# Optimization experiments

Hardware: AMD Instinct MI355X
Metric: run time of the kernel (lower is better)

The kernel has to match this reference:

```python
import jax, jax.numpy as jnp
import numpy as np

B, T, S, D = 4, 4, 128, 256  # batch, turns, seq_len, hidden_size
H = D  # GRU units == hidden_size


def setup_inputs() -> dict:
    key = jax.random.key(0)
    ks = jax.random.split(key, 8)
    sc = lambda *sh: float(np.sqrt(2.0 / sum(sh[:2]))) if len(sh) > 1 else 0.05
    return {
        "features": jax.random.normal(ks[0], (B, T, S, D), jnp.float32),
        "w1": jax.random.normal(ks[1], (D, D), jnp.float32) * sc(D, D),
        "w2": jax.random.normal(ks[2], (D, D), jnp.float32) * sc(D, D),
        "bias": jax.random.normal(ks[3], (D,), jnp.float32) * 0.05,
        "v3": jax.random.normal(ks[4], (D,), jnp.float32) * 0.05,
        "gru_kernel": jax.random.normal(ks[5], (2 * D, 3 * H), jnp.float32) * sc(2 * D, 3 * H),
        "gru_rec_kernel": jax.random.normal(ks[6], (H, 3 * H), jnp.float32) * sc(H, 3 * H),
        "gru_bias": jax.random.normal(ks[7], (2, 3 * H), jnp.float32) * 0.05,
    }


def _gru(x, kernel, rec_kernel, bias):
    # x: [N, S, 2D]; Keras GRU (reset_after=True, tanh/sigmoid), h0 = 0.
    b_in, b_rec = bias[0], bias[1]
    xp = x @ kernel + b_in               # [N, S, 3H] input projections
    xp_t = jnp.swapaxes(xp, 0, 1)        # [S, N, 3H]
    h0 = jnp.zeros((x.shape[0], H), x.dtype)

    def step(h, xt):
        rp = h @ rec_kernel + b_rec      # [N, 3H]
        xz, xr, xh = jnp.split(xt, 3, axis=-1)
        rz, rr, rh = jnp.split(rp, 3, axis=-1)
        z = jax.nn.sigmoid(xz + rz)
        r = jax.nn.sigmoid(xr + rr)
        hh = jnp.tanh(xh + r * rh)
        h_new = z * h + (1.0 - z) * hh
        return h_new, h_new

    _, ys = jax.lax.scan(step, h0, xp_t)  # ys: [S, N, H]
    return jnp.swapaxes(ys, 0, 1)         # [N, S, H]


def reference(features, w1, w2, bias, v3, gru_kernel, gru_rec_kernel, gru_bias):
    b, t, s, d = features.shape
    x = features.reshape(b * t, s, d)     # fold turns into batch (same per-utterance math)
    left = jnp.einsum('bsd,dt->bst', x, w1)
    right = jnp.einsum('bsd,dt->bst', x, w2)
    # additive (Bahdanau) scores: [N, s, s, d] intermediate
    temp = jnp.tanh(left[:, :, None, :] + right[:, None, :, :] + bias)
    score = jax.nn.softmax(jnp.einsum('bmnd,d->bmn', temp, v3), axis=-1)
    c = jnp.einsum('bmn,bnd->bmd', score, x)
    p = _gru(jnp.concatenate([x, c], axis=-1), gru_kernel, gru_rec_kernel, gru_bias)
    return p.reshape(b, t, s, H)
```

## Files before the change

kernel.cpp:

```cpp
#include <hip/hip_runtime.h>
#include <hip/hip_bf16.h>

typedef __attribute__((ext_vector_type(8))) short short8;
typedef __attribute__((ext_vector_type(4))) float floatx4;

#define NSEQ 16
#define SEQ 128
#define DIM 256
#define HID 256
#define K3H 768
#define K2D 512
#define LOG2E 1.442695041f
#define LOG2E2 2.885390082f
#define WS_STRIDE 772

__device__ __forceinline__ float frcp(float x) { return __builtin_amdgcn_rcpf(x); }
__device__ __forceinline__ unsigned short bf16bits(float v) {
    unsigned u = __builtin_bit_cast(unsigned, v);
    unsigned r = (u + 0x7FFFu + ((u >> 16) & 1u)) >> 16;
    return (unsigned short)r;
}
__device__ __forceinline__ void load_lds16(const float* gsrc, float* ldsbase) {
    __builtin_amdgcn_global_load_lds(
        (const __attribute__((address_space(1))) void*)gsrc,
        (__attribute__((address_space(3))) void*)ldsbase, 16, 0, 0);
}

__global__ __launch_bounds__(256) void k1_leftright(
        const float* __restrict__ x, const float* __restrict__ w1,
        const float* __restrict__ w2, float* __restrict__ left,
        float* __restrict__ right) {
    __shared__ __align__(16) float xs[8][DIM];
    const int tid = threadIdx.x;
    const int r0 = blockIdx.x * 8;
    #pragma unroll
    for (int i = 0; i < 8; ++i) xs[i][tid] = x[(r0 + i) * DIM + tid];
    __syncthreads();
    float accL[8], accR[8];
    #pragma unroll
    for (int i = 0; i < 8; ++i) { accL[i] = 0.f; accR[i] = 0.f; }
    #pragma unroll 4
    for (int d = 0; d < DIM; ++d) {
        float wa = w1[d * DIM + tid];
        float wb = w2[d * DIM + tid];
        #pragma unroll
        for (int i = 0; i < 8; ++i) {
            float xv = xs[i][d];
            accL[i] = fmaf(xv, wa, accL[i]);
            accR[i] = fmaf(xv, wb, accR[i]);
        }
    }
    #pragma unroll
    for (int i = 0; i < 8; ++i) {
        left[(r0 + i) * DIM + tid]  = accL[i] * LOG2E2;
        right[(r0 + i) * DIM + tid] = accR[i] * LOG2E2;
    }
}

__global__ __launch_bounds__(256) void k2_attn(
        const float* __restrict__ x, const float* __restrict__ left,
        const float* __restrict__ right, const float* __restrict__ bias,
        const float* __restrict__ v3, float* __restrict__ cout) {
    __shared__ __align__(16) float lm[8][DIM];
    __shared__ __align__(16) float v3s[DIM];
    __shared__ __align__(16) float P[8][SEQ];
    const int tid = threadIdx.x;
    const int b  = blockIdx.x >> 4;
    const int m0 = (blockIdx.x & 15) * 8;

    v3s[tid & 255] = v3[tid & 255];
    #pragma unroll
    for (int i = 0; i < 8; ++i)
        lm[i][tid] = left[(size_t)(b * SEQ + m0 + i) * DIM + tid] + bias[tid] * LOG2E2;
    __syncthreads();

    const int mi = tid >> 5;
    const int nl = tid & 31;
    float sacc[4] = {0.f, 0.f, 0.f, 0.f};
    const float4* lv4 = reinterpret_cast<const float4*>(lm[mi]);
    const float4* vv4 = reinterpret_cast<const float4*>(v3s);
    #pragma unroll 2
    for (int d4 = 0; d4 < DIM / 4; ++d4) {
        float4 lv = lv4[d4];
        float4 vv = vv4[d4];
        #pragma unroll
        for (int rep = 0; rep < 4; ++rep) {
            const int n = nl + rep * 32;
            float4 rv = reinterpret_cast<const float4*>(right + (size_t)(b * SEQ + n) * DIM)[d4];
            float t0 = 1.f - 2.f * frcp(1.f + __builtin_amdgcn_exp2f(lv.x + rv.x));
            float t1 = 1.f - 2.f * frcp(1.f + __builtin_amdgcn_exp2f(lv.y + rv.y));
            float t2 = 1.f - 2.f * frcp(1.f + __builtin_amdgcn_exp2f(lv.z + rv.z));
            float t3 = 1.f - 2.f * frcp(1.f + __builtin_amdgcn_exp2f(lv.w + rv.w));
            sacc[rep] = fmaf(t0, vv.x, sacc[rep]);
            sacc[rep] = fmaf(t1, vv.y, sacc[rep]);
            sacc[rep] = fmaf(t2, vv.z, sacc[rep]);
            sacc[rep] = fmaf(t3, vv.w, sacc[rep]);
        }
    }
    #pragma unroll
    for (int rep = 0; rep < 4; ++rep) P[mi][nl + rep * 32] = sacc[rep];
    __syncthreads();

    {
        const int w   = tid >> 6;
        const int lane = tid & 63;
        const int row = w * 2 + (lane >> 5);
        const int g   = lane & 31;
        float v0 = P[row][g], v1 = P[row][g + 32], v2 = P[row][g + 64], v3v = P[row][g + 96];
        float mx = fmaxf(fmaxf(v0, v1), fmaxf(v2, v3v));
        #pragma unroll
        for (int off = 16; off >= 1; off >>= 1) mx = fmaxf(mx, __shfl_xor(mx, off, 64));
        float e0 = __expf(v0 - mx), e1 = __expf(v1 - mx);
        float e2 = __expf(v2 - mx), e3 = __expf(v3v - mx);
        float sm = e0 + e1 + e2 + e3;
        #pragma unroll
        for (int off = 16; off >= 1; off >>= 1) sm += __shfl_xor(sm, off, 64);
        float inv = frcp(sm);
        P[row][g] = e0 * inv; P[row][g + 32] = e1 * inv;
        P[row][g + 64] = e2 * inv; P[row][g + 96] = e3 * inv;
    }
    __syncthreads();

    float acc[8];
    #pragma unroll
    for (int i = 0; i < 8; ++i) acc[i] = 0.f;
    const float* xb = x + (size_t)b * SEQ * DIM;
    for (int nc = 0; nc < SEQ / 4; ++nc) {
        float xv0 = xb[(nc * 4 + 0) * DIM + tid];
        float xv1 = xb[(nc * 4 + 1) * DIM + tid];
        float xv2 = xb[(nc * 4 + 2) * DIM + tid];
        float xv3 = xb[(nc * 4 + 3) * DIM + tid];
        #pragma unroll
        for (int i = 0; i < 8; ++i) {
            float4 pv = *reinterpret_cast<const float4*>(&P[i][nc * 4]);
            acc[i] = fmaf(pv.x, xv0, acc[i]);
            acc[i] = fmaf(pv.y, xv1, acc[i]);
            acc[i] = fmaf(pv.z, xv2, acc[i]);
            acc[i] = fmaf(pv.w, xv3, acc[i]);
        }
    }
    #pragma unroll
    for (int i = 0; i < 8; ++i)
        cout[(size_t)(b * SEQ + m0 + i) * DIM + tid] = acc[i];
}

__global__ __launch_bounds__(512) void k3_mfma(
        const float* __restrict__ x, const float* __restrict__ c,
        const float* __restrict__ gk, const float* __restrict__ gbias,
        float* __restrict__ xp) {
    __shared__ __align__(16) unsigned short As[64][72];
    __shared__ __align__(16) unsigned short Bs[192][72];
    const int tid  = threadIdx.x;
    const int lane = tid & 63;
    const int w    = tid >> 6;
    const int l15  = lane & 15;
    const int g4   = lane >> 4;
    const int wm   = w >> 2;
    const int wn   = w & 3;
    const int m0   = (blockIdx.x & 31) * 64;
    const int n0   = (blockIdx.x >> 5) * 192;

    floatx4 Cf[2][3];
    #pragma unroll
    for (int i = 0; i < 2; ++i)
        #pragma unroll
        for (int j = 0; j < 3; ++j) Cf[i][j] = (floatx4){0.f, 0.f, 0.f, 0.f};

    for (int ch = 0; ch < 8; ++ch) {
        const int kbase = ch * 64;
        #pragma unroll
        for (int q = 0; q < 2; ++q) {
            int fi = q * 512 + tid;
            int row = fi >> 4, kq = (fi & 15) << 2;
            int kg = kbase + kq;
            const float* src = (kg < 256) ? &x[(size_t)(m0 + row) * DIM + kg]
                                          : &c[(size_t)(m0 + row) * DIM + (kg - 256)];
            float4 v = *reinterpret_cast<const float4*>(src);
            unsigned short* dst = &As[row][kq];
            dst[0] = bf16bits(v.x); dst[1] = bf16bits(v.y);
            dst[2] = bf16bits(v.z); dst[3] = bf16bits(v.w);
        }
        #pragma unroll
        for (int q = 0; q < 6; ++q) {
            int fi = q * 512 + tid;
            int krow = fi / 48, nq = (fi % 48) << 2;
            float4 v = *reinterpret_cast<const float4*>(
                &gk[(size_t)(kbase + krow) * K3H + n0 + nq]);
            Bs[nq + 0][krow] = bf16bits(v.x);
            Bs[nq + 1][krow] = bf16bits(v.y);
            Bs[nq + 2][krow] = bf16bits(v.z);
            Bs[nq + 3][krow] = bf16bits(v.w);
        }
        __syncthreads();
        #pragma unroll
        for (int kk = 0; kk < 2; ++kk) {
            short8 af[2], bf[3];
            #pragma unroll
            for (int i = 0; i < 2; ++i)
                af[i] = *reinterpret_cast<const short8*>(&As[wm * 32 + i * 16 + l15][kk * 32 + g4 * 8]);
            #pragma unroll
            for (int j = 0; j < 3; ++j)
                bf[j] = *reinterpret_cast<const short8*>(&Bs[wn * 48 + j * 16 + l15][kk * 32 + g4 * 8]);
            #pragma unroll
            for (int i = 0; i < 2; ++i)
                #pragma unroll
                for (int j = 0; j < 3; ++j)
                    Cf[i][j] = __builtin_amdgcn_mfma_f32_16x16x32_bf16(af[i], bf[j], Cf[i][j], 0, 0, 0);
        }
        __syncthreads();
    }

    #pragma unroll
    for (int j = 0; j < 3; ++j) {
        const int nbase = n0 + wn * 48 + j * 16;
        const int col = nbase + l15;
        const float sc = (nbase >= 512) ? LOG2E2 : LOG2E;
        const float bv = ((col < 512) ? (gbias[col] + gbias[K3H + col]) : gbias[col]) * sc;
        #pragma unroll
        for (int i = 0; i < 2; ++i) {
            const int rbase = m0 + wm * 32 + i * 16 + g4 * 4;
            #pragma unroll
            for (int r = 0; r < 4; ++r)
                xp[(size_t)(rbase + r) * K3H + col] = fmaf(Cf[i][j][r], sc, bv);
        }
    }
}

__global__ __launch_bounds__(512) void k4_gru(
        const float* __restrict__ rec, const float* __restrict__ gbias,
        const float* __restrict__ xp, float* __restrict__ out) {
    __shared__ __align__(16) float ws[16 * WS_STRIDE];
    __shared__ __align__(16) float xq[3][K3H];
    __shared__ __align__(16) unsigned short hbf[2][HID];
    const int tid  = threadIdx.x;
    const int lane = tid & 63;
    const int wv   = tid >> 6;
    const int seq  = blockIdx.x;
    const int l15  = lane & 15;
    const int g4   = lane >> 4;

    short8 Bf[6][8];
    #pragma unroll
    for (int part = 0; part < 16; ++part) {
        #pragma unroll
        for (int q = 0; q < 6; ++q) {
            int fi = q * 512 + tid;
            int row = fi / 192, c4 = fi % 192;
            reinterpret_cast<float4*>(ws)[row * (WS_STRIDE / 4) + c4] =
                reinterpret_cast<const float4*>(rec + part * 16 * K3H)[fi];
        }
        __syncthreads();
        const int kc = part >> 1, half = part & 1;
        #pragma unroll
        for (int u = 0; u < 6; ++u) {
            const float sc = (u >= 4) ? LOG2E2 : LOG2E;
            const int col = (u >> 1) * 256 + (u & 1) * 16 + wv * 32 + l15;
            #pragma unroll
            for (int j = 0; j < 8; ++j) {
                int r = g4 * 8 + j;
                if ((r >> 4) == half)
                    Bf[u][kc][j] = (short)bf16bits(ws[(r & 15) * WS_STRIDE + col] * sc);
            }
        }
        __syncthreads();
    }

    const int dd = wv * 32 + (lane & 31);
    const float brh_l = gbias[K3H + 512 + dd] * LOG2E2;
    const int tsel = (lane >> 4) & 1;

    const float* xps = xp + (size_t)seq * SEQ * K3H;
    float* outs = out + (size_t)seq * SEQ * HID;

    float h = 0.f;
    if (tid < HID) hbf[0][tid] = 0;

    if (wv < 3) {
        load_lds16(xps + wv * 256 + (lane << 2),       &xq[0][wv * 256]);
        load_lds16(xps + K3H + wv * 256 + (lane << 2), &xq[1][wv * 256]);
    }
    asm volatile("s_waitcnt vmcnt(0)" ::: "memory");
    __syncthreads();

    int bc = 0, bn2 = 2;
    for (int s = 0; s < SEQ; ++s) {
        const int cb = s & 1, nb = cb ^ 1;

        const int sp = (s + 2 < SEQ) ? s + 2 : SEQ - 1;
        if (wv < 3)
            load_lds16(xps + (size_t)sp * K3H + wv * 256 + (lane << 2), &xq[bn2][wv * 256]);

        short8 av[8];
        #pragma unroll
        for (int kc = 0; kc < 8; ++kc)
            av[kc] = *reinterpret_cast<const short8*>(&hbf[cb][kc * 32 + g4 * 8]);
        const float xz = xq[bc][dd];
        const float xr = xq[bc][256 + dd];
        const float xh = xq[bc][512 + dd];

        floatx4 C[6];
        #pragma unroll
        for (int u = 0; u < 6; ++u) C[u] = (floatx4){0.f, 0.f, 0.f, 0.f};
        #pragma unroll
        for (int kc = 0; kc < 8; ++kc) {
            #pragma unroll
            for (int u = 0; u < 6; ++u)
                C[u] = __builtin_amdgcn_mfma_f32_16x16x32_bf16(av[kc], Bf[u][kc], C[u], 0, 0, 0);
        }
        if (lane < 32) {
            float rz = tsel ? C[1][0] : C[0][0];
            float rr = tsel ? C[3][0] : C[2][0];
            float rh = tsel ? C[5][0] : C[4][0];
            float z  = frcp(1.f + __builtin_amdgcn_exp2f(-(rz + xz)));
            float r  = frcp(1.f + __builtin_amdgcn_exp2f(-(rr + xr)));
            float th = fmaf(r, rh + brh_l, xh);
            float hh = 1.f - 2.f * frcp(1.f + __builtin_amdgcn_exp2f(th));
            h = hh + z * (h - hh);
            hbf[nb][dd] = bf16bits(h);
            outs[s * HID + dd] = h;
        }
        asm volatile("s_waitcnt vmcnt(3) lgkmcnt(0)\n\ts_barrier" ::: "memory");

        bc  = (bc == 2)  ? 0 : bc + 1;
        bn2 = (bn2 == 2) ? 0 : bn2 + 1;
    }
}

extern "C" void kernel_launch(void* const* d_in, const int* in_sizes, int n_in,
                              void* d_out, int out_size, void* d_ws, size_t ws_size,
                              hipStream_t stream) {
    const float* feat = (const float*)d_in[0];
    const float* w1   = (const float*)d_in[1];
    const float* w2   = (const float*)d_in[2];
    const float* bias = (const float*)d_in[3];
    const float* v3   = (const float*)d_in[4];
    const float* gk   = (const float*)d_in[5];
    const float* grk  = (const float*)d_in[6];
    const float* gb   = (const float*)d_in[7];
    float* out = (float*)d_out;

    char* wsb = (char*)d_ws;
    float* left  = (float*)(wsb);
    float* right = (float*)(wsb + (size_t)2 * 1024 * 1024);
    float* cbuf  = (float*)(wsb + (size_t)4 * 1024 * 1024);
    float* xp    = (float*)(wsb + (size_t)6 * 1024 * 1024);

    k1_leftright<<<2048 / 8, 256, 0, stream>>>(feat, w1, w2, left, right);
    k2_attn<<<NSEQ * 16, 256, 0, stream>>>(feat, left, right, bias, v3, cbuf);
    k3_mfma<<<128, 512, 0, stream>>>(feat, cbuf, gk, gb, xp);
    k4_gru<<<NSEQ, 512, 0, stream>>>(grk, gb, xp, out);
}
```

Before: 241.9 us.

## Process two GRU sequences per block to interleave independent recurrences

The GRU kernel now handles two sequences per workgroup, launching half as many blocks. Each step runs two independent MFMA chains on the same register-resident recurrent weights, so one sequence's latency can be hidden behind the other's. The per-step critical path grows, since each wave issues twice the MFMAs and activations, and only 8 blocks run on a large GPU, which lowers parallelism. The wait count is adjusted for the extra outstanding stores and loads per step.

```diff
diff --git a/kernel.cpp b/kernel.cpp
--- a/kernel.cpp
+++ b/kernel.cpp
@@ -230,12 +230,13 @@
         const float* __restrict__ rec, const float* __restrict__ gbias,
         const float* __restrict__ xp, float* __restrict__ out) {
     __shared__ __align__(16) float ws[16 * WS_STRIDE];
-    __shared__ __align__(16) float xq[3][K3H];
-    __shared__ __align__(16) unsigned short hbf[2][HID];
+    __shared__ __align__(16) float xqA[3][K3H];
+    __shared__ __align__(16) float xqB[3][K3H];
+    __shared__ __align__(16) unsigned short hbfA[2][HID];
+    __shared__ __align__(16) unsigned short hbfB[2][HID];
     const int tid  = threadIdx.x;
     const int lane = tid & 63;
     const int wv   = tid >> 6;
-    const int seq  = blockIdx.x;
     const int l15  = lane & 15;
     const int g4   = lane >> 4;
 
@@ -269,15 +270,22 @@
     const float brh_l = gbias[K3H + 512 + dd] * LOG2E2;
     const int tsel = (lane >> 4) & 1;
 
-    const float* xps = xp + (size_t)seq * SEQ * K3H;
-    float* outs = out + (size_t)seq * SEQ * HID;
-
-    float h = 0.f;
-    if (tid < HID) hbf[0][tid] = 0;
+    const int sA = blockIdx.x * 2, sB = sA + 1;
+    const float* xpsA = xp + (size_t)sA * SEQ * K3H;
+    const float* xpsB = xp + (size_t)sB * SEQ * K3H;
+    float* outsA = out + (size_t)sA * SEQ * HID;
+    float* outsB = out + (size_t)sB * SEQ * HID;
+
+    float hA = 0.f, hB = 0.f;
+    if (tid < HID) { hbfA[0][tid] = 0; hbfB[0][tid] = 0; }
 
     if (wv < 3) {
-        load_lds16(xps + wv * 256 + (lane << 2),       &xq[0][wv * 256]);
-        load_lds16(xps + K3H + wv * 256 + (lane << 2), &xq[1][wv * 256]);
+        load_lds16(xpsA + wv * 256 + (lane << 2),       &xqA[0][wv * 256]);
+        load_lds16(xpsA + K3H + wv * 256 + (lane << 2), &xqA[1][wv * 256]);
+    } else if (wv < 6) {
+        const int w3 = wv - 3;
+        load_lds16(xpsB + w3 * 256 + (lane << 2),       &xqB[0][w3 * 256]);
+        load_lds16(xpsB + K3H + w3 * 256 + (lane << 2), &xqB[1][w3 * 256]);
     }
     asm volatile("s_waitcnt vmcnt(0)" ::: "memory");
     __syncthreads();
@@ -288,38 +296,68 @@
 
         const int sp = (s + 2 < SEQ) ? s + 2 : SEQ - 1;
         if (wv < 3)
-            load_lds16(xps + (size_t)sp * K3H + wv * 256 + (lane << 2), &xq[bn2][wv * 256]);
-
-        short8 av[8];
+            load_lds16(xpsA + (size_t)sp * K3H + wv * 256 + (lane << 2), &xqA[bn2][wv * 256]);
+        else if (wv < 6)
+            load_lds16(xpsB + (size_t)sp * K3H + (wv - 3) * 256 + (lane << 2), &xqB[bn2][(wv - 3) * 256]);
+
+        short8 avA[8];
         #pragma unroll
         for (int kc = 0; kc < 8; ++kc)
-            av[kc] = *reinterpret_cast<const short8*>(&hbf[cb][kc * 32 + g4 * 8]);
-        const float xz = xq[bc][dd];
-        const float xr = xq[bc][256 + dd];
-        const float xh = xq[bc][512 + dd];
-
-        floatx4 C[6];
-        #pragma unroll
-        for (int u = 0; u < 6; ++u) C[u] = (floatx4){0.f, 0.f, 0.f, 0.f};
+            avA[kc] = *reinterpret_cast<const short8*>(&hbfA[cb][kc * 32 + g4 * 8]);
+        const float xzA = xqA[bc][dd];
+        const float xrA = xqA[bc][256 + dd];
+        const float xhA = xqA[bc][512 + dd];
+        floatx4 CA[6];
+        #pragma unroll
+        for (int u = 0; u < 6; ++u) CA[u] = (floatx4){0.f, 0.f, 0.f, 0.f};
         #pragma unroll
         for (int kc = 0; kc < 8; ++kc) {
             #pragma unroll
             for (int u = 0; u < 6; ++u)
-                C[u] = __builtin_amdgcn_mfma_f32_16x16x32_bf16(av[kc], Bf[u][kc], C[u], 0, 0, 0);
-        }
+                CA[u] = __builtin_amdgcn_mfma_f32_16x16x32_bf16(avA[kc], Bf[u][kc], CA[u], 0, 0, 0);
+        }
+        const float rzA = tsel ? CA[1][0] : CA[0][0];
+        const float rrA = tsel ? CA[3][0] : CA[2][0];
+        const float rhA = tsel ? CA[5][0] : CA[4][0];
+
+        short8 avB[8];
+        #pragma unroll
+        for (int kc = 0; kc < 8; ++kc)
+            avB[kc] = *reinterpret_cast<const short8*>(&hbfB[cb][kc * 32 + g4 * 8]);
+        const float xzB = xqB[bc][dd];
+        const float xrB = xqB[bc][256 + dd];
+        const float xhB = xqB[bc][512 + dd];
+        floatx4 CB[6];
+        #pragma unroll
+        for (int u = 0; u < 6; ++u) CB[u] = (floatx4){0.f, 0.f, 0.f, 0.f};
+        #pragma unroll
+        for (int kc = 0; kc < 8; ++kc) {
+            #pragma unroll
+            for (int u = 0; u < 6; ++u)
+                CB[u] = __builtin_amdgcn_mfma_f32_16x16x32_bf16(avB[kc], Bf[u][kc], CB[u], 0, 0, 0);
+        }
+        const float rzB = tsel ? CB[1][0] : CB[0][0];
+        const float rrB = tsel ? CB[3][0] : CB[2][0];
+        const float rhB = tsel ? CB[5][0] : CB[4][0];
+
         if (lane < 32) {
-            float rz = tsel ? C[1][0] : C[0][0];
-            float rr = tsel ? C[3][0] : C[2][0];
-            float rh = tsel ? C[5][0] : C[4][0];
-            float z  = frcp(1.f + __builtin_amdgcn_exp2f(-(rz + xz)));
-            float r  = frcp(1.f + __builtin_amdgcn_exp2f(-(rr + xr)));
-            float th = fmaf(r, rh + brh_l, xh);
-            float hh = 1.f - 2.f * frcp(1.f + __builtin_amdgcn_exp2f(th));
-            h = hh + z * (h - hh);
-            hbf[nb][dd] = bf16bits(h);
-            outs[s * HID + dd] = h;
-        }
-        asm volatile("s_waitcnt vmcnt(3) lgkmcnt(0)\n\ts_barrier" ::: "memory");
+            float zA  = frcp(1.f + __builtin_amdgcn_exp2f(-(rzA + xzA)));
+            float rA  = frcp(1.f + __builtin_amdgcn_exp2f(-(rrA + xrA)));
+            float thA = fmaf(rA, rhA + brh_l, xhA);
+            float hhA = 1.f - 2.f * frcp(1.f + __builtin_amdgcn_exp2f(thA));
+            hA = hhA + zA * (hA - hhA);
+            hbfA[nb][dd] = bf16bits(hA);
+            outsA[s * HID + dd] = hA;
+
+            float zB  = frcp(1.f + __builtin_amdgcn_exp2f(-(rzB + xzB)));
+            float rB  = frcp(1.f + __builtin_amdgcn_exp2f(-(rrB + xrB)));
+            float thB = fmaf(rB, rhB + brh_l, xhB);
+            float hhB = 1.f - 2.f * frcp(1.f + __builtin_amdgcn_exp2f(thB));
+            hB = hhB + zB * (hB - hhB);
+            hbfB[nb][dd] = bf16bits(hB);
+            outsB[s * HID + dd] = hB;
+        }
+        asm volatile("s_waitcnt vmcnt(5) lgkmcnt(0)\n\ts_barrier" ::: "memory");
 
         bc  = (bc == 2)  ? 0 : bc + 1;
         bn2 = (bn2 == 2) ? 0 : bn2 + 1;
@@ -348,5 +386,5 @@
     k1_leftright<<<2048 / 8, 256, 0, stream>>>(feat, w1, w2, left, right);
     k2_attn<<<NSEQ * 16, 256, 0, stream>>>(feat, left, right, bias, v3, cbuf);
     k3_mfma<<<128, 512, 0, stream>>>(feat, cbuf, gk, gb, xp);
-    k4_gru<<<NSEQ, 512, 0, stream>>>(grk, gb, xp, out);
-}
+    k4_gru<<<NSEQ / 2, 512, 0, stream>>>(grk, gb, xp, out);
+}
```

Result: slower. 348.2 us (+44.0%).
